# Optimization experiments

Measured on AMD Instinct MI355X. Metric: run time of the kernel, lower is better.

The kernel has to match this reference:

```python
import jax, jax.numpy as jnp
import numpy as np

HEADS = 8
DIM_HEAD = 64
QUERY_DIM = 1024
CONTEXT_DIM = 768
INNER = HEADS * DIM_HEAD  # 512


def setup_inputs() -> dict:
    key = jax.random.key(0)
    ks = jax.random.split(key, 7)
    B, Sq, Skv = 4, 4096, 1024
    x = jax.random.normal(ks[0], (B, Sq, QUERY_DIM), dtype=jnp.float32)
    context = jax.random.normal(ks[1], (B, Skv, CONTEXT_DIM), dtype=jnp.float32)
    # nn.Linear(in, out) weights stored as [out, in]; we use [in, out] for x @ W
    Wq = jax.random.normal(ks[2], (QUERY_DIM, INNER), dtype=jnp.float32) * (QUERY_DIM ** -0.5)
    Wk = jax.random.normal(ks[3], (CONTEXT_DIM, INNER), dtype=jnp.float32) * (CONTEXT_DIM ** -0.5)
    Wv = jax.random.normal(ks[4], (CONTEXT_DIM, INNER), dtype=jnp.float32) * (CONTEXT_DIM ** -0.5)
    Wo = jax.random.normal(ks[5], (INNER, QUERY_DIM), dtype=jnp.float32) * (INNER ** -0.5)
    bo = jax.random.normal(ks[6], (QUERY_DIM,), dtype=jnp.float32) * 0.01
    return {"x": x, "context": context, "Wq": Wq, "Wk": Wk, "Wv": Wv, "Wo": Wo, "bo": bo}


def reference(x, context, Wq, Wk, Wv, Wo, bo):
    B, Sq, _ = x.shape
    h, d = HEADS, DIM_HEAD
    scale = d ** -0.5
    # project and split heads: [B, S, h*d] -> [B, h, S, d]
    q = (x @ Wq).reshape(B, Sq, h, d).transpose(0, 2, 1, 3)
    k = (context @ Wk).reshape(B, -1, h, d).transpose(0, 2, 1, 3)
    v = (context @ Wv).reshape(B, -1, h, d).transpose(0, 2, 1, 3)
    # the torch chunked loop is exactly full softmax attention (softmax is row-wise)
    scores = jnp.einsum('bhid,bhjd->bhij', q, k) * scale
    attn = jax.nn.softmax(scores, axis=-1)
    out = jnp.einsum('bhij,bhjd->bhid', attn, v)  # [B, h, Sq, d]
    out = out.transpose(0, 2, 1, 3).reshape(B, Sq, h * d)
    return out @ Wo + bo
```

## Files before the change

### kernel.cpp

```cpp
#include <hip/hip_runtime.h>

#define SQ 4096
#define SKV 1024
#define BATCH 4
#define NH 8
#define DH 64
#define QD 1024
#define CD 768
#define INNER 512

typedef _Float16 half8 __attribute__((ext_vector_type(8)));
typedef _Float16 half4v __attribute__((ext_vector_type(4)));
typedef float floatx4 __attribute__((ext_vector_type(4)));

#define MFMA16(a, b, c) __builtin_amdgcn_mfma_f32_16x16x32_f16(a, b, c, 0, 0, 0)

#define GLD16(gptr, lptr)                                                            \
  __builtin_amdgcn_global_load_lds(                                                  \
      (const __attribute__((address_space(1))) unsigned int*)(const void*)(gptr),    \
      (__attribute__((address_space(3))) unsigned int*)(void*)(lptr), 16, 0, 0)

__global__ __launch_bounds__(256) void transpose_all(const float* __restrict__ Wq,
                                                     const float* __restrict__ Wk,
                                                     const float* __restrict__ Wv,
                                                     const float* __restrict__ Wo,
                                                     _Float16* __restrict__ wqt,
                                                     _Float16* __restrict__ wkvt,
                                                     _Float16* __restrict__ wot) {
  __shared__ float tile[32][33];
  const int z = blockIdx.z;
  const float* src; _Float16* dst; int R, C;
  if (z == 0)      { src = Wq; dst = wqt;                        R = QD;    C = INNER; }
  else if (z == 1) { src = Wk; dst = wkvt;                       R = CD;    C = INNER; }
  else if (z == 2) { src = Wv; dst = wkvt + (size_t)INNER * CD;  R = CD;    C = INNER; }
  else             { src = Wo; dst = wot;                        R = INNER; C = QD;   }
  const int c0 = blockIdx.x * 32, r0 = blockIdx.y * 32;
  if (c0 >= C || r0 >= R) return;
  const int tx = threadIdx.x & 31, ty = threadIdx.x >> 5;
#pragma unroll
  for (int i = 0; i < 32; i += 8)
    tile[ty + i][tx] = src[(size_t)(r0 + ty + i) * C + c0 + tx];
  __syncthreads();
#pragma unroll
  for (int i = 0; i < 32; i += 8)
    dst[(size_t)(c0 + ty + i) * R + r0 + tx] = (_Float16)tile[tx][ty + i];
}

template <int MODE, int AF32>
__global__ __launch_bounds__(256) void gemm128(const void* __restrict__ Aany,
                                               const _Float16* __restrict__ Bt,
                                               void* __restrict__ Cout,
                                               void* __restrict__ Cout2,
                                               const float* __restrict__ bias,
                                               int M, int N, int K) {
  __shared__ char AsRaw[AF32 ? 128 * 32 * 4 : 128 * 32 * 2];
  __shared__ _Float16 Bs[128 * 32];
  float* As32 = (float*)AsRaw;
  _Float16* As16 = (_Float16*)AsRaw;

  const int tid = threadIdx.x;
  const int wave = tid >> 6, lane = tid & 63;
  const int quad = lane >> 4, l16 = lane & 15;
  const int wm = (wave >> 1) * 64, wn = (wave & 1) * 64;
  const size_t n0 = (size_t)blockIdx.x * 128, m0 = (size_t)blockIdx.y * 128;

  floatx4 acc[4][4] = {};

  const float* a32g = (const float*)Aany + (m0 + (tid >> 3)) * (size_t)K + (tid & 7) * 4;
  const _Float16* a16g = (const _Float16*)Aany + (m0 + (tid >> 2)) * (size_t)K + (tid & 3) * 8;
  const _Float16* bg = Bt + (n0 + (tid >> 2)) * (size_t)K + (tid & 3) * 8;

  for (int k0 = 0; k0 < K; k0 += 32) {
    __syncthreads();
    if (AF32) {
#pragma unroll
      for (int j = 0; j < 4; ++j)
        GLD16(a32g + k0 + (size_t)j * 32 * K, As32 + tid * 4 + j * 1024);
    } else {
#pragma unroll
      for (int j = 0; j < 2; ++j)
        GLD16(a16g + k0 + (size_t)j * 64 * K, As16 + tid * 8 + j * 2048);
    }
#pragma unroll
    for (int j = 0; j < 2; ++j)
      GLD16(bg + k0 + (size_t)j * 64 * K, Bs + tid * 8 + j * 2048);
    __syncthreads();

    half8 af[4], bf[4];
#pragma unroll
    for (int mt = 0; mt < 4; ++mt) {
      const int row = wm + mt * 16 + l16;
      if (AF32) {
        floatx4 x0 = *(const floatx4*)(As32 + row * 32 + quad * 8);
        floatx4 x1 = *(const floatx4*)(As32 + row * 32 + quad * 8 + 4);
        half8 t;
#pragma unroll
        for (int i = 0; i < 4; ++i) { t[i] = (_Float16)x0[i]; t[4 + i] = (_Float16)x1[i]; }
        af[mt] = t;
      } else {
        af[mt] = *(const half8*)(As16 + row * 32 + quad * 8);
      }
    }
#pragma unroll
    for (int nt = 0; nt < 4; ++nt)
      bf[nt] = *(const half8*)(Bs + (wn + nt * 16 + l16) * 32 + quad * 8);
#pragma unroll
    for (int mt = 0; mt < 4; ++mt)
#pragma unroll
      for (int nt = 0; nt < 4; ++nt)
        acc[mt][nt] = MFMA16(af[mt], bf[nt], acc[mt][nt]);
  }

  if (MODE == 0 || MODE == 3) {
    _Float16* C = (_Float16*)Cout;
    const float sc = (MODE == 3) ? 0.125f : 1.0f;
#pragma unroll
    for (int mt = 0; mt < 4; ++mt) {
      const size_t row = m0 + wm + mt * 16 + quad * 4;
#pragma unroll
      for (int nt = 0; nt < 4; ++nt) {
        const size_t col = n0 + wn + nt * 16 + l16;
#pragma unroll
        for (int r = 0; r < 4; ++r)
          C[(row + r) * N + col] = (_Float16)(acc[mt][nt][r] * sc);
      }
    }
  } else if (MODE == 4) {
    if (n0 < INNER) {
      _Float16* C = (_Float16*)Cout;
#pragma unroll
      for (int mt = 0; mt < 4; ++mt) {
        const size_t row = m0 + wm + mt * 16 + quad * 4;
#pragma unroll
        for (int nt = 0; nt < 4; ++nt) {
          const size_t col = n0 + wn + nt * 16 + l16;
#pragma unroll
          for (int r = 0; r < 4; ++r)
            C[(row + r) * INNER + col] = (_Float16)acc[mt][nt][r];
        }
      }
    } else {
      _Float16* C = (_Float16*)Cout2;
      const int b = (int)(m0 >> 10);
#pragma unroll
      for (int mt = 0; mt < 4; ++mt) {
        const int kvb = (int)(m0 & 1023) + wm + mt * 16 + quad * 4;
#pragma unroll
        for (int nt = 0; nt < 4; ++nt) {
          const int col = (int)(n0 - INNER + wn + nt * 16 + l16);
          const int h = col >> 6, d = col & 63;
          half4v pk;
#pragma unroll
          for (int r = 0; r < 4; ++r) pk[r] = (_Float16)acc[mt][nt][r];
          *(half4v*)(C + (size_t)((b * NH + h) * DH + d) * SKV + kvb) = pk;
        }
      }
    }
  } else {
    float* C = (float*)Cout;
#pragma unroll
    for (int mt = 0; mt < 4; ++mt) {
      const size_t row = m0 + wm + mt * 16 + quad * 4;
#pragma unroll
      for (int nt = 0; nt < 4; ++nt) {
        const size_t col = n0 + wn + nt * 16 + l16;
        const float bb = bias[col];
#pragma unroll
        for (int r = 0; r < 4; ++r)
          C[(row + r) * N + col] = acc[mt][nt][r] + bb;
      }
    }
  }
}

__global__ __launch_bounds__(256, 3) void flash_attn4(const _Float16* __restrict__ Q,
                                                      const _Float16* __restrict__ Kp,
                                                      const _Float16* __restrict__ Vt,
                                                      _Float16* __restrict__ O) {
  constexpr int KST = 72;
  constexpr int VST = 136;
  constexpr int PST = 40;
  __shared__ _Float16 Ks[128 * KST];
  __shared__ _Float16 Vs[64 * VST];
  __shared__ _Float16 Ps[4][32 * PST];
  const int tid = threadIdx.x;
  const int wave = tid >> 6, lane = tid & 63;
  const int quad = lane >> 4, l16 = lane & 15;
  const int qblk = blockIdx.x, bh = blockIdx.y;
  const int b = bh >> 3, h = bh & 7;

  const size_t qrow0 = (size_t)b * SQ + qblk * 128 + wave * 32;
  const _Float16* qptr = Q + qrow0 * INNER + h * DH;
  const _Float16* kbase = Kp + (size_t)b * SKV * INNER + h * DH;
  const _Float16* vbase = Vt + (size_t)bh * DH * SKV;
  _Float16* pw = Ps[wave];

  const int krow = tid >> 3, kcol = (tid & 7) * 8;
  const int vrow = tid >> 4, vcol = (tid & 15) * 8;

  half8 aq[2][2];
#pragma unroll
  for (int hh = 0; hh < 2; ++hh) {
    aq[hh][0] = *(const half8*)(qptr + (size_t)(hh * 16 + l16) * INNER + quad * 8);
    aq[hh][1] = *(const half8*)(qptr + (size_t)(hh * 16 + l16) * INNER + 32 + quad * 8);
  }

  floatx4 o[2][4] = {};
  float lsum[2][4] = {};

  half8 kpre[4], vpre[4];
#pragma unroll
  for (int i = 0; i < 4; ++i)
    kpre[i] = *(const half8*)(kbase + (size_t)(krow + i * 32) * INNER + kcol);
#pragma unroll
  for (int i = 0; i < 4; ++i)
    vpre[i] = *(const half8*)(vbase + (size_t)(vrow + i * 16) * SKV + vcol);

  for (int t = 0; t < SKV / 128; ++t) {
    __syncthreads();
#pragma unroll
    for (int i = 0; i < 4; ++i)
      *(half8*)(Ks + (krow + i * 32) * KST + kcol) = kpre[i];
#pragma unroll
    for (int i = 0; i < 4; ++i)
      *(half8*)(Vs + (vrow + i * 16) * VST + vcol) = vpre[i];
    __syncthreads();

    if (t < SKV / 128 - 1) {
      const int kv1 = (t + 1) * 128;
#pragma unroll
      for (int i = 0; i < 4; ++i)
        kpre[i] = *(const half8*)(kbase + (size_t)(kv1 + krow + i * 32) * INNER + kcol);
#pragma unroll
      for (int i = 0; i < 4; ++i)
        vpre[i] = *(const half8*)(vbase + (size_t)(vrow + i * 16) * SKV + kv1 + vcol);
    }

#pragma unroll
    for (int c = 0; c < 4; ++c) {
      floatx4 s[2][2];
#pragma unroll
      for (int j2 = 0; j2 < 2; ++j2) {
        const _Float16* kj = Ks + (c * 32 + j2 * 16 + l16) * KST + quad * 8;
        half8 k0 = *(const half8*)kj;
        half8 k1 = *(const half8*)(kj + 32);
#pragma unroll
        for (int hh = 0; hh < 2; ++hh) {
          floatx4 acc = {0.f, 0.f, 0.f, 0.f};
          acc = MFMA16(aq[hh][0], k0, acc);
          acc = MFMA16(aq[hh][1], k1, acc);
          s[hh][j2] = acc;
        }
      }
#pragma unroll
      for (int hh = 0; hh < 2; ++hh)
#pragma unroll
        for (int j2 = 0; j2 < 2; ++j2)
#pragma unroll
          for (int r = 0; r < 4; ++r) {
            float p = __expf(s[hh][j2][r]);
            lsum[hh][r] += p;
            pw[(hh * 16 + quad * 4 + r) * PST + j2 * 16 + l16] = (_Float16)p;
          }
      __builtin_amdgcn_wave_barrier();
      half8 ap0 = *(const half8*)(pw + (size_t)l16 * PST + quad * 8);
      half8 ap1 = *(const half8*)(pw + (size_t)(16 + l16) * PST + quad * 8);
#pragma unroll
      for (int nt = 0; nt < 4; ++nt) {
        half8 bv = *(const half8*)(Vs + (size_t)(nt * 16 + l16) * VST + c * 32 + quad * 8);
        o[0][nt] = MFMA16(ap0, bv, o[0][nt]);
        o[1][nt] = MFMA16(ap1, bv, o[1][nt]);
      }
      __builtin_amdgcn_wave_barrier();
    }
  }

  float inv[2][4];
#pragma unroll
  for (int hh = 0; hh < 2; ++hh)
#pragma unroll
    for (int r = 0; r < 4; ++r) {
      float v = lsum[hh][r];
      v += __shfl_xor(v, 1);
      v += __shfl_xor(v, 2);
      v += __shfl_xor(v, 4);
      v += __shfl_xor(v, 8);
      inv[hh][r] = 1.0f / v;
    }
  _Float16* op = O + qrow0 * INNER + h * DH;
#pragma unroll
  for (int hh = 0; hh < 2; ++hh)
#pragma unroll
    for (int nt = 0; nt < 4; ++nt)
#pragma unroll
      for (int r = 0; r < 4; ++r)
        op[(size_t)(hh * 16 + quad * 4 + r) * INNER + nt * 16 + l16] =
            (_Float16)(o[hh][nt][r] * inv[hh][r]);
}

extern "C" void kernel_launch(void* const* d_in, const int* in_sizes, int n_in,
                              void* d_out, int out_size, void* d_ws, size_t ws_size,
                              hipStream_t stream) {
  const float* x   = (const float*)d_in[0];
  const float* ctx = (const float*)d_in[1];
  const float* Wq  = (const float*)d_in[2];
  const float* Wk  = (const float*)d_in[3];
  const float* Wv  = (const float*)d_in[4];
  const float* Wo  = (const float*)d_in[5];
  const float* bo  = (const float*)d_in[6];
  float* out = (float*)d_out;

  _Float16* ws = (_Float16*)d_ws;
  _Float16* wqt  = ws;
  _Float16* wkvt = wqt + (size_t)INNER * QD;
  _Float16* wot  = wkvt + (size_t)2 * INNER * CD;
  _Float16* qh   = wot + (size_t)QD * INNER;
  _Float16* kh   = qh + (size_t)BATCH * SQ * INNER;
  _Float16* vth  = kh + (size_t)BATCH * SKV * INNER;
  _Float16* aoh  = vth + (size_t)BATCH * SKV * INNER;

  transpose_all<<<dim3(32, 32, 4), 256, 0, stream>>>(Wq, Wk, Wv, Wo, wqt, wkvt, wot);

  gemm128<3, 1><<<dim3(INNER / 128, BATCH * SQ / 128), 256, 0, stream>>>(
      (const void*)x, wqt, (void*)qh, nullptr, nullptr, BATCH * SQ, INNER, QD);
  gemm128<4, 1><<<dim3(2 * INNER / 128, BATCH * SKV / 128), 256, 0, stream>>>(
      (const void*)ctx, wkvt, (void*)kh, (void*)vth, nullptr, BATCH * SKV, 2 * INNER, CD);

  flash_attn4<<<dim3(SQ / 128, BATCH * NH), 256, 0, stream>>>(qh, kh, vth, aoh);

  gemm128<2, 0><<<dim3(QD / 128, BATCH * SQ / 128), 256, 0, stream>>>(
      (const void*)aoh, wot, (void*)out, nullptr, bo, BATCH * SQ, QD, INNER);
}
```

Baseline: 296.6 us.

## Keep attention probabilities in registers and read V directly from global

The attention kernel now computes transposed scores (K as the A operand) so the probabilities can be repacked into the PV MFMA operand through lane shuffles instead of a round trip through per-wave shared memory. V is no longer staged in LDS and is read directly from global memory each chunk. The log2(e) factor is folded into the Q projection scale so exp2 replaces exp. Blocks are remapped to a flat, interleaved grid and the occupancy hint goes from 3 to 4 blocks. This trades LDS traffic and footprint for extra shuffles and uncoalesced-ish global V reads that must hit cache.

```diff
diff --git a/kernel.cpp b/kernel.cpp
--- a/kernel.cpp
+++ b/kernel.cpp
@@ -12,6 +12,7 @@
 typedef _Float16 half8 __attribute__((ext_vector_type(8)));
 typedef _Float16 half4v __attribute__((ext_vector_type(4)));
 typedef float floatx4 __attribute__((ext_vector_type(4)));
+typedef unsigned int uint4v __attribute__((ext_vector_type(4)));
 
 #define MFMA16(a, b, c) __builtin_amdgcn_mfma_f32_16x16x32_f16(a, b, c, 0, 0, 0)
 
@@ -113,7 +114,7 @@
 
   if (MODE == 0 || MODE == 3) {
     _Float16* C = (_Float16*)Cout;
-    const float sc = (MODE == 3) ? 0.125f : 1.0f;
+    const float sc = (MODE == 3) ? 0.125f * 1.44269504088896f : 1.0f;
 #pragma unroll
     for (int mt = 0; mt < 4; ++mt) {
       const size_t row = m0 + wm + mt * 16 + quad * 4;
@@ -173,30 +174,27 @@
   }
 }
 
-__global__ __launch_bounds__(256, 3) void flash_attn4(const _Float16* __restrict__ Q,
+__global__ __launch_bounds__(256, 4) void flash_attn5(const _Float16* __restrict__ Q,
                                                       const _Float16* __restrict__ Kp,
                                                       const _Float16* __restrict__ Vt,
                                                       _Float16* __restrict__ O) {
   constexpr int KST = 72;
-  constexpr int VST = 136;
-  constexpr int PST = 40;
   __shared__ _Float16 Ks[128 * KST];
-  __shared__ _Float16 Vs[64 * VST];
-  __shared__ _Float16 Ps[4][32 * PST];
   const int tid = threadIdx.x;
   const int wave = tid >> 6, lane = tid & 63;
   const int quad = lane >> 4, l16 = lane & 15;
-  const int qblk = blockIdx.x, bh = blockIdx.y;
+
+  const int flat = blockIdx.x;
+  const int nf = (flat & 7) * 128 + (flat >> 3);
+  const int qblk = nf & 31, bh = nf >> 5;
   const int b = bh >> 3, h = bh & 7;
 
   const size_t qrow0 = (size_t)b * SQ + qblk * 128 + wave * 32;
   const _Float16* qptr = Q + qrow0 * INNER + h * DH;
   const _Float16* kbase = Kp + (size_t)b * SKV * INNER + h * DH;
   const _Float16* vbase = Vt + (size_t)bh * DH * SKV;
-  _Float16* pw = Ps[wave];
 
   const int krow = tid >> 3, kcol = (tid & 7) * 8;
-  const int vrow = tid >> 4, vcol = (tid & 15) * 8;
 
   half8 aq[2][2];
 #pragma unroll
@@ -206,87 +204,100 @@
   }
 
   floatx4 o[2][4] = {};
-  float lsum[2][4] = {};
-
-  half8 kpre[4], vpre[4];
+  float lsum[2] = {0.f, 0.f};
+
+  half8 kpre[4];
 #pragma unroll
   for (int i = 0; i < 4; ++i)
     kpre[i] = *(const half8*)(kbase + (size_t)(krow + i * 32) * INNER + kcol);
-#pragma unroll
-  for (int i = 0; i < 4; ++i)
-    vpre[i] = *(const half8*)(vbase + (size_t)(vrow + i * 16) * SKV + vcol);
 
   for (int t = 0; t < SKV / 128; ++t) {
     __syncthreads();
 #pragma unroll
     for (int i = 0; i < 4; ++i)
       *(half8*)(Ks + (krow + i * 32) * KST + kcol) = kpre[i];
-#pragma unroll
-    for (int i = 0; i < 4; ++i)
-      *(half8*)(Vs + (vrow + i * 16) * VST + vcol) = vpre[i];
     __syncthreads();
-
     if (t < SKV / 128 - 1) {
       const int kv1 = (t + 1) * 128;
 #pragma unroll
       for (int i = 0; i < 4; ++i)
         kpre[i] = *(const half8*)(kbase + (size_t)(kv1 + krow + i * 32) * INNER + kcol);
-#pragma unroll
-      for (int i = 0; i < 4; ++i)
-        vpre[i] = *(const half8*)(vbase + (size_t)(vrow + i * 16) * SKV + kv1 + vcol);
-    }
+    }
+    const _Float16* vt0 = vbase + t * 128;
 
 #pragma unroll
     for (int c = 0; c < 4; ++c) {
-      floatx4 s[2][2];
-#pragma unroll
-      for (int j2 = 0; j2 < 2; ++j2) {
-        const _Float16* kj = Ks + (c * 32 + j2 * 16 + l16) * KST + quad * 8;
-        half8 k0 = *(const half8*)kj;
-        half8 k1 = *(const half8*)(kj + 32);
-#pragma unroll
-        for (int hh = 0; hh < 2; ++hh) {
-          floatx4 acc = {0.f, 0.f, 0.f, 0.f};
-          acc = MFMA16(aq[hh][0], k0, acc);
-          acc = MFMA16(aq[hh][1], k1, acc);
-          s[hh][j2] = acc;
+      half8 bv[4];
+#pragma unroll
+      for (int nt = 0; nt < 4; ++nt)
+        bv[nt] = *(const half8*)(vt0 + (size_t)(nt * 16 + l16) * SKV + c * 32 + quad * 8);
+
+      const _Float16* kj = Ks + (c * 32 + l16) * KST + quad * 8;
+      half8 k0a = *(const half8*)kj;
+      half8 k0b = *(const half8*)(kj + 32);
+      half8 k1a = *(const half8*)(kj + 16 * KST);
+      half8 k1b = *(const half8*)(kj + 16 * KST + 32);
+
+#pragma unroll
+      for (int hh = 0; hh < 2; ++hh) {
+        floatx4 st0 = {0.f, 0.f, 0.f, 0.f}, st1 = {0.f, 0.f, 0.f, 0.f};
+        st0 = MFMA16(k0a, aq[hh][0], st0);
+        st0 = MFMA16(k0b, aq[hh][1], st0);
+        st1 = MFMA16(k1a, aq[hh][0], st1);
+        st1 = MFMA16(k1b, aq[hh][1], st1);
+
+        float p0[4], p1[4];
+#pragma unroll
+        for (int r = 0; r < 4; ++r) {
+          p0[r] = __builtin_exp2f(st0[r]);
+          p1[r] = __builtin_exp2f(st1[r]);
         }
-      }
-#pragma unroll
-      for (int hh = 0; hh < 2; ++hh)
-#pragma unroll
-        for (int j2 = 0; j2 < 2; ++j2)
-#pragma unroll
-          for (int r = 0; r < 4; ++r) {
-            float p = __expf(s[hh][j2][r]);
-            lsum[hh][r] += p;
-            pw[(hh * 16 + quad * 4 + r) * PST + j2 * 16 + l16] = (_Float16)p;
-          }
-      __builtin_amdgcn_wave_barrier();
-      half8 ap0 = *(const half8*)(pw + (size_t)l16 * PST + quad * 8);
-      half8 ap1 = *(const half8*)(pw + (size_t)(16 + l16) * PST + quad * 8);
-#pragma unroll
-      for (int nt = 0; nt < 4; ++nt) {
-        half8 bv = *(const half8*)(Vs + (size_t)(nt * 16 + l16) * VST + c * 32 + quad * 8);
-        o[0][nt] = MFMA16(ap0, bv, o[0][nt]);
-        o[1][nt] = MFMA16(ap1, bv, o[1][nt]);
-      }
-      __builtin_amdgcn_wave_barrier();
-    }
-  }
-
+        lsum[hh] += (p0[0] + p0[1] + p0[2] + p0[3]) + (p1[0] + p1[1] + p1[2] + p1[3]);
+
+        unsigned pk00 = __builtin_bit_cast(unsigned, __builtin_amdgcn_cvt_pkrtz(p0[0], p0[1]));
+        unsigned pk01 = __builtin_bit_cast(unsigned, __builtin_amdgcn_cvt_pkrtz(p0[2], p0[3]));
+        unsigned pk10 = __builtin_bit_cast(unsigned, __builtin_amdgcn_cvt_pkrtz(p1[0], p1[1]));
+        unsigned pk11 = __builtin_bit_cast(unsigned, __builtin_amdgcn_cvt_pkrtz(p1[2], p1[3]));
+
+        const int bsel = ((lane & 16) << 1) + l16;
+        const bool jlo = (lane & 32) == 0;
+        unsigned s00 = __shfl(pk00, bsel);
+        unsigned s10 = __shfl(pk10, bsel);
+        unsigned s01 = __shfl(pk01, bsel);
+        unsigned s11 = __shfl(pk11, bsel);
+        unsigned s00b = __shfl(pk00, bsel + 16);
+        unsigned s10b = __shfl(pk10, bsel + 16);
+        unsigned s01b = __shfl(pk01, bsel + 16);
+        unsigned s11b = __shfl(pk11, bsel + 16);
+        uint4v wv;
+        wv[0] = jlo ? s00 : s10;
+        wv[1] = jlo ? s01 : s11;
+        wv[2] = jlo ? s00b : s10b;
+        wv[3] = jlo ? s01b : s11b;
+        half8 ap = __builtin_bit_cast(half8, wv);
+
+#pragma unroll
+        for (int nt = 0; nt < 4; ++nt)
+          o[hh][nt] = MFMA16(ap, bv[nt], o[hh][nt]);
+      }
+    }
+  }
+
+  float tot[2];
+#pragma unroll
+  for (int hh = 0; hh < 2; ++hh) {
+    float v = lsum[hh];
+    v += __shfl_xor(v, 16);
+    v += __shfl_xor(v, 32);
+    tot[hh] = v;
+  }
   float inv[2][4];
 #pragma unroll
   for (int hh = 0; hh < 2; ++hh)
 #pragma unroll
-    for (int r = 0; r < 4; ++r) {
-      float v = lsum[hh][r];
-      v += __shfl_xor(v, 1);
-      v += __shfl_xor(v, 2);
-      v += __shfl_xor(v, 4);
-      v += __shfl_xor(v, 8);
-      inv[hh][r] = 1.0f / v;
-    }
+    for (int r = 0; r < 4; ++r)
+      inv[hh][r] = 1.0f / __shfl(tot[hh], quad * 4 + r);
+
   _Float16* op = O + qrow0 * INNER + h * DH;
 #pragma unroll
   for (int hh = 0; hh < 2; ++hh)
@@ -326,7 +337,7 @@
   gemm128<4, 1><<<dim3(2 * INNER / 128, BATCH * SKV / 128), 256, 0, stream>>>(
       (const void*)ctx, wkvt, (void*)kh, (void*)vth, nullptr, BATCH * SKV, 2 * INNER, CD);
 
-  flash_attn4<<<dim3(SQ / 128, BATCH * NH), 256, 0, stream>>>(qh, kh, vth, aoh);
+  flash_attn5<<<dim3(BATCH * NH * SQ / 128), 256, 0, stream>>>(qh, kh, vth, aoh);
 
   gemm128<2, 0><<<dim3(QD / 128, BATCH * SQ / 128), 256, 0, stream>>>(
       (const void*)aoh, wot, (void*)out, nullptr, bo, BATCH * SQ, QD, INNER);
```

After: 375.4 us. +26.6%, slower.
